# Kernel tuning notes

Measured on AMD Instinct MI355X. Metric: run time of the kernel, lower is better.

## Reference

```python
import jax, jax.numpy as jnp
import numpy as np

HEADS = 16
HEAD_DIM = 64
TOKEN_DIM = 1024
INNER = HEADS * HEAD_DIM


def setup_inputs() -> dict:
    key = jax.random.key(0)
    k1, k2, k3, k4 = jax.random.split(key, 4)
    x = jax.random.normal(k1, (2, 2048, TOKEN_DIM), dtype=jnp.float32)
    # nn.Linear(token_dim, inner*3, bias=False): weight [3*inner, token_dim]
    w_qkv = jax.random.normal(k2, (3 * INNER, TOKEN_DIM), dtype=jnp.float32) * (TOKEN_DIM ** -0.5)
    # nn.Linear(inner, token_dim): weight [token_dim, inner], bias [token_dim]
    w_out = jax.random.normal(k3, (TOKEN_DIM, INNER), dtype=jnp.float32) * (INNER ** -0.5)
    b_out = jax.random.normal(k4, (TOKEN_DIM,), dtype=jnp.float32) * 0.01
    return {"x": x, "w_qkv": w_qkv, "w_out": w_out, "b_out": b_out}


def reference(x, w_qkv, w_out, b_out):
    b, n, _ = x.shape
    scale = HEAD_DIM ** -0.5
    qkv = x @ w_qkv.T                                  # [b, n, 3*inner]
    q, k, v = jnp.split(qkv, 3, axis=-1)
    def split_heads(t):
        return t.reshape(b, n, HEADS, HEAD_DIM).transpose(0, 2, 1, 3)  # [b,h,n,d]
    q, k, v = split_heads(q), split_heads(k), split_heads(v)
    dot = jnp.einsum('bhtd,bhsd->bhts', q, k) * scale  # [b,h,n,n]
    attn = jax.nn.softmax(dot, axis=-1)
    out = jnp.einsum('bhts,bhsd->bhtd', attn, v)       # [b,h,n,d]
    out = out.transpose(0, 2, 1, 3).reshape(b, n, INNER)
    return out @ w_out.T + b_out
```

## Files before the change

### kernel.cpp

```cpp
#include <hip/hip_runtime.h>
#include <hip/hip_bf16.h>

typedef short short4v __attribute__((ext_vector_type(4)));
typedef short short8 __attribute__((ext_vector_type(8)));
typedef float float4v __attribute__((ext_vector_type(4)));

#define HEADS 16
#define HDIM 64
#define TOKDIM 1024
#define SEQ 2048
#define BATCH 2
#define BH (BATCH*HEADS)
#define MROWS (BATCH*SEQ)

__device__ __forceinline__ short f2b(float f) {
    __hip_bfloat16 h = __float2bfloat16(f);
    return *reinterpret_cast<short*>(&h);
}
__device__ __forceinline__ float b2f(short s) {
    __hip_bfloat16 h;
    *reinterpret_cast<short*>(&h) = s;
    return __bfloat162float(h);
}
__device__ __forceinline__ short8 load8_f32_bf16(const float* __restrict__ p) {
    float4v a = *(const float4v*)p;
    float4v b = *(const float4v*)(p + 4);
    short8 r;
    r[0]=f2b(a[0]); r[1]=f2b(a[1]); r[2]=f2b(a[2]); r[3]=f2b(a[3]);
    r[4]=f2b(b[0]); r[5]=f2b(b[1]); r[6]=f2b(b[2]); r[7]=f2b(b[3]);
    return r;
}
__device__ __forceinline__ int packrn(float a, float b) {
    unsigned ua = __float_as_uint(a) + 0x8000u;
    unsigned ub = __float_as_uint(b) + 0x8000u;
    return (int)__builtin_amdgcn_perm(ub, ua, 0x07060302u);
}
__device__ __forceinline__ float hexp2(float x) {
    return __builtin_amdgcn_exp2f(x);
}

__device__ __forceinline__ void stage16(const void* g, void* l) {
    __builtin_amdgcn_global_load_lds((const __attribute__((address_space(1))) void*)g,
                                     (__attribute__((address_space(3))) void*)l, 16, 0, 0);
}

__global__ __launch_bounds__(256)
void cvt_bf16(const float* __restrict__ x,  short* __restrict__ xb,  int n8x,
              const float* __restrict__ wq, short* __restrict__ wqb, int n8q,
              const float* __restrict__ wo, short* __restrict__ wob, int n8o)
{
    int i = blockIdx.x*256 + threadIdx.x;
    const float* s; short* d; int off;
    if (i < n8x)                  { s = x;  d = xb;  off = i; }
    else if (i < n8x + n8q)       { s = wq; d = wqb; off = i - n8x; }
    else if (i < n8x + n8q + n8o) { s = wo; d = wob; off = i - n8x - n8q; }
    else return;
    *(short8*)&d[(size_t)off*8] = load8_f32_bf16(&s[(size_t)off*8]);
}

template<int ABF16>
__global__ __launch_bounds__(256)
void gemm_qkv(const void* __restrict__ Ap, const short* __restrict__ Wq,
              short* __restrict__ Qo, short* __restrict__ Ko, short* __restrict__ Vto)
{
    __shared__ __align__(16) short As[128*32];
    __shared__ __align__(16) short Bs[128*32];
    const int tid  = threadIdx.x;
    const int lane = tid & 63;
    const int wave = tid >> 6;
    const int wm = wave >> 1, wn = wave & 1;
    const int m0 = blockIdx.x * 128;
    const int n0 = blockIdx.y * 128;
    const int col16 = lane & 15, quad = lane >> 4;

    const int srow = lane >> 2;
    const int scol = (lane & 3) * 8;

    float4v acc[4][4];
    #pragma unroll
    for (int i=0;i<4;i++)
        #pragma unroll
        for (int j=0;j<4;j++) acc[i][j] = (float4v){0.f,0.f,0.f,0.f};

    for (int k0 = 0; k0 < TOKDIM; k0 += 32) {
        __syncthreads();
        if (ABF16) {
            const short* A = (const short*)Ap;
            #pragma unroll
            for (int j=0;j<2;++j) {
                const int rb = (wave*2 + j) * 16;
                stage16(&A[(size_t)(m0 + rb + srow)*TOKDIM + k0 + scol], &As[rb*32]);
            }
        } else {
            const float* A = (const float*)Ap;
            #pragma unroll
            for (int s=0;s<2;++s) {
                int blk = tid + s*256;
                int r = blk >> 2, kb = blk & 3;
                *(short8*)&As[r*32 + kb*8] = load8_f32_bf16(&A[(size_t)(m0+r)*TOKDIM + k0 + kb*8]);
            }
        }
        #pragma unroll
        for (int j=0;j<2;++j) {
            const int rb = (wave*2 + j) * 16;
            stage16(&Wq[(size_t)(n0 + rb + srow)*TOKDIM + k0 + scol], &Bs[rb*32]);
        }
        __syncthreads();

        short8 af[4], bfr[4];
        #pragma unroll
        for (int i=0;i<4;i++) af[i]  = *(const short8*)&As[(wm*64 + i*16 + col16)*32 + quad*8];
        #pragma unroll
        for (int j=0;j<4;j++) bfr[j] = *(const short8*)&Bs[(wn*64 + j*16 + col16)*32 + quad*8];
        #pragma unroll
        for (int i=0;i<4;i++)
            #pragma unroll
            for (int j=0;j<4;j++)
                acc[i][j] = __builtin_amdgcn_mfma_f32_16x16x32_bf16(af[i], bfr[j], acc[i][j], 0,0,0);
    }

    #pragma unroll
    for (int i=0;i<4;i++)
        #pragma unroll
        for (int j=0;j<4;j++) {
            const int n = n0 + wn*64 + j*16 + col16;
            const int part = n >> 10;
            const int h = (n & 1023) >> 6;
            const int d = n & 63;
            const int mb = m0 + wm*64 + i*16 + quad*4;
            const int b = mb >> 11;
            const int t = mb & 2047;
            if (part == 2) {
                union { short4v s; int2 i2; } w;
                #pragma unroll
                for (int r=0;r<4;r++) w.s[r] = f2b(acc[i][j][r]);
                *(int2*)&Vto[((size_t)(b*HEADS + h)*HDIM + d)*SEQ + t] = w.i2;
            } else {
                short* dst = (part == 0) ? Qo : Ko;
                #pragma unroll
                for (int r=0;r<4;r++)
                    dst[((size_t)(b*HEADS + h)*SEQ + t + r)*HDIM + d] = f2b(acc[i][j][r]);
            }
        }
}

__global__ __launch_bounds__(256)
void gemm_out(const short* __restrict__ A, const short* __restrict__ W,
              const float* __restrict__ bias, float* __restrict__ C)
{
    __shared__ __align__(16) short As[64*32];
    __shared__ __align__(16) short Bs[128*32];
    const int tid  = threadIdx.x;
    const int lane = tid & 63;
    const int wave = tid >> 6;
    const int wm = wave >> 1, wn = wave & 1;
    const int m0 = blockIdx.x * 64;
    const int n0 = blockIdx.y * 128;
    const int col16 = lane & 15, quad = lane >> 4;

    const int srow = lane >> 2;
    const int scol = (lane & 3) * 8;

    float4v acc[2][4];
    #pragma unroll
    for (int i=0;i<2;i++)
        #pragma unroll
        for (int j=0;j<4;j++) acc[i][j] = (float4v){0.f,0.f,0.f,0.f};

    for (int k0 = 0; k0 < TOKDIM; k0 += 32) {
        __syncthreads();
        {
            const int rb = wave * 16;
            stage16(&A[(size_t)(m0 + rb + srow)*TOKDIM + k0 + scol], &As[rb*32]);
        }
        #pragma unroll
        for (int j=0;j<2;++j) {
            const int rb = (wave*2 + j) * 16;
            stage16(&W[(size_t)(n0 + rb + srow)*TOKDIM + k0 + scol], &Bs[rb*32]);
        }
        __syncthreads();

        short8 af[2], bfr[4];
        #pragma unroll
        for (int i=0;i<2;i++) af[i]  = *(const short8*)&As[(wm*32 + i*16 + col16)*32 + quad*8];
        #pragma unroll
        for (int j=0;j<4;j++) bfr[j] = *(const short8*)&Bs[(wn*64 + j*16 + col16)*32 + quad*8];
        #pragma unroll
        for (int i=0;i<2;i++)
            #pragma unroll
            for (int j=0;j<4;j++)
                acc[i][j] = __builtin_amdgcn_mfma_f32_16x16x32_bf16(af[i], bfr[j], acc[i][j], 0,0,0);
    }

    #pragma unroll
    for (int i=0;i<2;i++)
        #pragma unroll
        for (int j=0;j<4;j++) {
            const int n = n0 + wn*64 + j*16 + col16;
            const float bn = bias[n];
            #pragma unroll
            for (int r=0;r<4;r++) {
                const int m = m0 + wm*32 + i*16 + quad*4 + r;
                C[(size_t)m*TOKDIM + n] = acc[i][j][r] + bn;
            }
        }
}

#define AQB 128
#define KT  64
#define VLD 72

__global__ __launch_bounds__(256, 4)
void attn_kernel(const short* __restrict__ Q, const short* __restrict__ K,
                 const short* __restrict__ Vt, short* __restrict__ AO)
{
    __shared__ __align__(16) short Ks[2][KT*VLD];
    __shared__ __align__(16) short Vs[2][HDIM*VLD];

    const int tid   = threadIdx.x;
    const int lane  = tid & 63;
    const int wave  = tid >> 6;
    const int col16 = lane & 15, quad = lane >> 4;
    const int bh = blockIdx.y;
    const int qb = blockIdx.x*AQB + wave*32;

    const short* Qb = Q  + (size_t)bh*SEQ*HDIM;
    const short* Kb = K  + (size_t)bh*SEQ*HDIM;
    const short* Vb = Vt + (size_t)bh*HDIM*SEQ;

    const int sr = tid >> 2;
    const int sc = (tid & 3) * 16;
    const int rho = sr & 31;
    const int kslot = (sr & 32) + ((rho & 4) << 2) + ((rho & 24) >> 1) + (rho & 3);

    const float qscale = 0.125f * 1.44269504088896f;
    short8 qf[2][2];
    #pragma unroll
    for (int qg=0; qg<2; ++qg)
        #pragma unroll
        for (int kh=0; kh<2; ++kh) {
            short8 raw = *(const short8*)&Qb[(size_t)(qb+qg*16+col16)*HDIM + kh*32 + quad*8];
            #pragma unroll
            for (int j=0;j<8;++j) raw[j] = f2b(b2f(raw[j]) * qscale);
            qf[qg][kh] = raw;
        }

    float4v o[2][4];
    #pragma unroll
    for (int qg=0;qg<2;qg++)
        #pragma unroll
        for (int dt=0;dt<4;dt++) o[qg][dt] = (float4v){0.f,0.f,0.f,0.f};
    float lsum[2] = {0.f, 0.f};

    {
        short8 k0 = *(const short8*)&Kb[(size_t)sr*HDIM + sc];
        short8 k1 = *(const short8*)&Kb[(size_t)sr*HDIM + sc + 8];
        short8 v0 = *(const short8*)&Vb[(size_t)sr*SEQ + sc];
        short8 v1 = *(const short8*)&Vb[(size_t)sr*SEQ + sc + 8];
        *(short8*)&Ks[0][kslot*VLD + sc]     = k0;
        *(short8*)&Ks[0][kslot*VLD + sc + 8] = k1;
        *(short8*)&Vs[0][sr*VLD + sc]        = v0;
        *(short8*)&Vs[0][sr*VLD + sc + 8]    = v1;
    }
    __syncthreads();

    const int NT = SEQ / KT;
    for (int tile = 0; tile < NT; ++tile) {
        const int buf = tile & 1;

        short8 nk0, nk1, nv0, nv1;
        const bool more = (tile + 1 < NT);
        if (more) {
            const int s1 = (tile + 1) * KT;
            nk0 = *(const short8*)&Kb[(size_t)(s1 + sr)*HDIM + sc];
            nk1 = *(const short8*)&Kb[(size_t)(s1 + sr)*HDIM + sc + 8];
            nv0 = *(const short8*)&Vb[(size_t)sr*SEQ + s1 + sc];
            nv1 = *(const short8*)&Vb[(size_t)sr*SEQ + s1 + sc + 8];
        }

        #pragma unroll
        for (int kk = 0; kk < 2; ++kk) {
            short8 ka[2][2];
            #pragma unroll
            for (int nt=0; nt<2; ++nt)
                #pragma unroll
                for (int kh=0; kh<2; ++kh)
                    ka[nt][kh] = *(const short8*)&Ks[buf][(kk*32 + nt*16 + col16)*VLD + kh*32 + quad*8];
            short8 va[4];
            #pragma unroll
            for (int dt=0; dt<4; ++dt)
                va[dt] = *(const short8*)&Vs[buf][(dt*16 + col16)*VLD + kk*32 + quad*8];

            #pragma unroll
            for (int qg=0; qg<2; ++qg) {
                float4v st[2];
                #pragma unroll
                for (int nt=0; nt<2; ++nt) {
                    float4v z = (float4v){0.f,0.f,0.f,0.f};
                    z = __builtin_amdgcn_mfma_f32_16x16x32_bf16(ka[nt][0], qf[qg][0], z, 0,0,0);
                    z = __builtin_amdgcn_mfma_f32_16x16x32_bf16(ka[nt][1], qf[qg][1], z, 0,0,0);
                    st[nt] = z;
                }
                union { int i[4]; short8 s8; } pb;
                float p00 = hexp2(st[0][0]), p01 = hexp2(st[0][1]);
                float p02 = hexp2(st[0][2]), p03 = hexp2(st[0][3]);
                float p10 = hexp2(st[1][0]), p11 = hexp2(st[1][1]);
                float p12 = hexp2(st[1][2]), p13 = hexp2(st[1][3]);
                lsum[qg] += ((p00+p01) + (p02+p03)) + ((p10+p11) + (p12+p13));
                pb.i[0] = packrn(p00, p01); pb.i[1] = packrn(p02, p03);
                pb.i[2] = packrn(p10, p11); pb.i[3] = packrn(p12, p13);

                #pragma unroll
                for (int dt=0; dt<4; ++dt)
                    o[qg][dt] = __builtin_amdgcn_mfma_f32_16x16x32_bf16(va[dt], pb.s8, o[qg][dt], 0,0,0);
            }
        }

        if (more) {
            const int nb = buf ^ 1;
            *(short8*)&Ks[nb][kslot*VLD + sc]     = nk0;
            *(short8*)&Ks[nb][kslot*VLD + sc + 8] = nk1;
            *(short8*)&Vs[nb][sr*VLD + sc]        = nv0;
            *(short8*)&Vs[nb][sr*VLD + sc + 8]    = nv1;
        }
        __syncthreads();
    }

    #pragma unroll
    for (int qg=0; qg<2; ++qg) {
        lsum[qg] += __shfl_xor(lsum[qg], 16);
        lsum[qg] += __shfl_xor(lsum[qg], 32);
    }

    const int b = bh >> 4, h = bh & 15;
    #pragma unroll
    for (int qg=0; qg<2; ++qg) {
        const float inv = 1.0f / lsum[qg];
        const int t = qb + qg*16 + col16;
        #pragma unroll
        for (int dt=0; dt<4; ++dt) {
            union { short4v s; int2 i2; } w;
            #pragma unroll
            for (int r=0;r<4;++r) w.s[r] = f2b(o[qg][dt][r] * inv);
            *(int2*)&AO[((size_t)(b*SEQ + t))*TOKDIM + h*64 + dt*16 + quad*4] = w.i2;
        }
    }
}

extern "C" void kernel_launch(void* const* d_in, const int* in_sizes, int n_in,
                              void* d_out, int out_size, void* d_ws, size_t ws_size,
                              hipStream_t stream)
{
    const float* x    = (const float*)d_in[0];
    const float* wqkv = (const float*)d_in[1];
    const float* wout = (const float*)d_in[2];
    const float* bout = (const float*)d_in[3];
    float* out = (float*)d_out;

    char* ws = (char*)d_ws;
    const size_t SZ   = (size_t)BH*SEQ*HDIM*sizeof(short);
    const size_t WQB  = (size_t)3*TOKDIM*TOKDIM*sizeof(short);
    const size_t WOB  = (size_t)TOKDIM*TOKDIM*sizeof(short);
    const size_t NEED_FULL = SZ + WQB + WOB + 3*SZ;
    const bool full = ws_size >= NEED_FULL;

    short *Xb, *Wqb, *Wob, *Qt, *Kt, *Vt, *AO;
    if (full) {
        Xb  = (short*)ws;
        Wqb = (short*)(ws + SZ);
        Wob = (short*)(ws + SZ + WQB);
        Qt  = (short*)(ws + SZ + WQB + WOB);
        Kt  = Qt + SZ/2;
        Vt  = Kt + SZ/2;
        AO  = Xb;
    } else {
        Xb  = nullptr;
        Wqb = (short*)ws;
        Wob = (short*)(ws + WQB);
        Qt  = (short*)(ws + WQB + WOB);
        Kt  = Qt + SZ/2;
        Vt  = Kt + SZ/2;
        AO  = Vt + SZ/2;
    }

    const int n8x = full ? (BATCH*SEQ*TOKDIM)/8 : 0;
    const int n8q = (3*TOKDIM*TOKDIM)/8;
    const int n8o = (TOKDIM*TOKDIM)/8;
    const int cvt_blocks = (n8x + n8q + n8o + 255) / 256;
    cvt_bf16<<<cvt_blocks, 256, 0, stream>>>(x, Xb, n8x, wqkv, Wqb, n8q, wout, Wob, n8o);

    if (full)
        gemm_qkv<1><<<dim3(MROWS/128, (3*TOKDIM)/128), 256, 0, stream>>>(
            (const void*)Xb, Wqb, Qt, Kt, Vt);
    else
        gemm_qkv<0><<<dim3(MROWS/128, (3*TOKDIM)/128), 256, 0, stream>>>(
            (const void*)x, Wqb, Qt, Kt, Vt);

    attn_kernel<<<dim3(SEQ/AQB, BH), 256, 0, stream>>>(Qt, Kt, Vt, AO);

    gemm_out<<<dim3(MROWS/64, TOKDIM/128), 256, 0, stream>>>(AO, Wob, bout, out);
}
```

Before: 184.6 us.

## Split KV sequence across wave pairs in attention with 64-query waves and LDS merge

Each attention block now has two wave pairs. Each pair processes half of the key/value sequence, and each wave handles 64 queries instead of 32. This doubles the reuse of every K/V fragment loaded from LDS across query groups. Double buffering is replaced by a single buffer per half, with two barriers per tile. The partial outputs and row sums are merged through LDS at the end. Register pressure rises (launch bounds drop to 2 blocks per SM), and the load-to-compute overlap is weaker because of the extra barrier.

```diff
diff --git a/kernel.cpp b/kernel.cpp
--- a/kernel.cpp
+++ b/kernel.cpp
@@ -209,73 +209,77 @@
 #define AQB 128
 #define KT  64
 #define VLD 72
-
-__global__ __launch_bounds__(256, 4)
+#define NTH 16
+
+__global__ __launch_bounds__(256, 2)
 void attn_kernel(const short* __restrict__ Q, const short* __restrict__ K,
                  const short* __restrict__ Vt, short* __restrict__ AO)
 {
-    __shared__ __align__(16) short Ks[2][KT*VLD];
-    __shared__ __align__(16) short Vs[2][HDIM*VLD];
+    __shared__ __align__(16) short SL[2*2*KT*VLD];
 
     const int tid   = threadIdx.x;
     const int lane  = tid & 63;
     const int wave  = tid >> 6;
     const int col16 = lane & 15, quad = lane >> 4;
-    const int bh = blockIdx.y;
-    const int qb = blockIdx.x*AQB + wave*32;
+    const int bh  = blockIdx.y;
+    const int qh  = wave & 1;
+    const int kh2 = wave >> 1;
+    const int qb  = blockIdx.x*AQB + qh*64;
 
     const short* Qb = Q  + (size_t)bh*SEQ*HDIM;
     const short* Kb = K  + (size_t)bh*SEQ*HDIM;
     const short* Vb = Vt + (size_t)bh*HDIM*SEQ;
 
-    const int sr = tid >> 2;
-    const int sc = (tid & 3) * 16;
+    short* Kcs = &SL[kh2*2*KT*VLD];
+    short* Vcs = Kcs + KT*VLD;
+
+    const int local = tid & 127;
+    const int sr = local >> 1;
+    const int sc = (local & 1) * 32;
     const int rho = sr & 31;
     const int kslot = (sr & 32) + ((rho & 4) << 2) + ((rho & 24) >> 1) + (rho & 3);
+    const int kbase = kh2 * 1024;
 
     const float qscale = 0.125f * 1.44269504088896f;
-    short8 qf[2][2];
-    #pragma unroll
-    for (int qg=0; qg<2; ++qg)
-        #pragma unroll
-        for (int kh=0; kh<2; ++kh) {
-            short8 raw = *(const short8*)&Qb[(size_t)(qb+qg*16+col16)*HDIM + kh*32 + quad*8];
+    short8 qf[4][2];
+    #pragma unroll
+    for (int qg=0; qg<4; ++qg)
+        #pragma unroll
+        for (int kk=0; kk<2; ++kk) {
+            short8 raw = *(const short8*)&Qb[(size_t)(qb+qg*16+col16)*HDIM + kk*32 + quad*8];
             #pragma unroll
             for (int j=0;j<8;++j) raw[j] = f2b(b2f(raw[j]) * qscale);
-            qf[qg][kh] = raw;
-        }
-
-    float4v o[2][4];
-    #pragma unroll
-    for (int qg=0;qg<2;qg++)
+            qf[qg][kk] = raw;
+        }
+
+    float4v o[4][4];
+    #pragma unroll
+    for (int qg=0;qg<4;qg++)
         #pragma unroll
         for (int dt=0;dt<4;dt++) o[qg][dt] = (float4v){0.f,0.f,0.f,0.f};
-    float lsum[2] = {0.f, 0.f};
+    float lsum[4] = {0.f,0.f,0.f,0.f};
 
     {
-        short8 k0 = *(const short8*)&Kb[(size_t)sr*HDIM + sc];
-        short8 k1 = *(const short8*)&Kb[(size_t)sr*HDIM + sc + 8];
-        short8 v0 = *(const short8*)&Vb[(size_t)sr*SEQ + sc];
-        short8 v1 = *(const short8*)&Vb[(size_t)sr*SEQ + sc + 8];
-        *(short8*)&Ks[0][kslot*VLD + sc]     = k0;
-        *(short8*)&Ks[0][kslot*VLD + sc + 8] = k1;
-        *(short8*)&Vs[0][sr*VLD + sc]        = v0;
-        *(short8*)&Vs[0][sr*VLD + sc + 8]    = v1;
+        #pragma unroll
+        for (int i=0;i<4;++i) {
+            *(short8*)&Kcs[kslot*VLD + sc + i*8] =
+                *(const short8*)&Kb[(size_t)(kbase + sr)*HDIM + sc + i*8];
+            *(short8*)&Vcs[sr*VLD + sc + i*8] =
+                *(const short8*)&Vb[(size_t)sr*SEQ + kbase + sc + i*8];
+        }
     }
     __syncthreads();
 
-    const int NT = SEQ / KT;
-    for (int tile = 0; tile < NT; ++tile) {
-        const int buf = tile & 1;
-
-        short8 nk0, nk1, nv0, nv1;
-        const bool more = (tile + 1 < NT);
+    for (int t = 0; t < NTH; ++t) {
+        short8 nk[4], nv[4];
+        const bool more = (t + 1 < NTH);
         if (more) {
-            const int s1 = (tile + 1) * KT;
-            nk0 = *(const short8*)&Kb[(size_t)(s1 + sr)*HDIM + sc];
-            nk1 = *(const short8*)&Kb[(size_t)(s1 + sr)*HDIM + sc + 8];
-            nv0 = *(const short8*)&Vb[(size_t)sr*SEQ + s1 + sc];
-            nv1 = *(const short8*)&Vb[(size_t)sr*SEQ + s1 + sc + 8];
+            const int g1 = kbase + (t+1)*KT;
+            #pragma unroll
+            for (int i=0;i<4;++i) {
+                nk[i] = *(const short8*)&Kb[(size_t)(g1 + sr)*HDIM + sc + i*8];
+                nv[i] = *(const short8*)&Vb[(size_t)sr*SEQ + g1 + sc + i*8];
+            }
         }
 
         #pragma unroll
@@ -285,14 +289,14 @@
             for (int nt=0; nt<2; ++nt)
                 #pragma unroll
                 for (int kh=0; kh<2; ++kh)
-                    ka[nt][kh] = *(const short8*)&Ks[buf][(kk*32 + nt*16 + col16)*VLD + kh*32 + quad*8];
+                    ka[nt][kh] = *(const short8*)&Kcs[(kk*32 + nt*16 + col16)*VLD + kh*32 + quad*8];
             short8 va[4];
             #pragma unroll
             for (int dt=0; dt<4; ++dt)
-                va[dt] = *(const short8*)&Vs[buf][(dt*16 + col16)*VLD + kk*32 + quad*8];
-
-            #pragma unroll
-            for (int qg=0; qg<2; ++qg) {
+                va[dt] = *(const short8*)&Vcs[(dt*16 + col16)*VLD + kk*32 + quad*8];
+
+            #pragma unroll
+            for (int qg=0; qg<4; ++qg) {
                 float4v st[2];
                 #pragma unroll
                 for (int nt=0; nt<2; ++nt) {
@@ -316,33 +320,50 @@
             }
         }
 
+        __syncthreads();
         if (more) {
-            const int nb = buf ^ 1;
-            *(short8*)&Ks[nb][kslot*VLD + sc]     = nk0;
-            *(short8*)&Ks[nb][kslot*VLD + sc + 8] = nk1;
-            *(short8*)&Vs[nb][sr*VLD + sc]        = nv0;
-            *(short8*)&Vs[nb][sr*VLD + sc + 8]    = nv1;
-        }
-        __syncthreads();
-    }
-
-    #pragma unroll
-    for (int qg=0; qg<2; ++qg) {
+            #pragma unroll
+            for (int i=0;i<4;++i) {
+                *(short8*)&Kcs[kslot*VLD + sc + i*8] = nk[i];
+                *(short8*)&Vcs[sr*VLD + sc + i*8]    = nv[i];
+            }
+            __syncthreads();
+        }
+    }
+
+    #pragma unroll
+    for (int qg=0; qg<4; ++qg) {
         lsum[qg] += __shfl_xor(lsum[qg], 16);
         lsum[qg] += __shfl_xor(lsum[qg], 32);
     }
 
-    const int b = bh >> 4, h = bh & 15;
-    #pragma unroll
-    for (int qg=0; qg<2; ++qg) {
-        const float inv = 1.0f / lsum[qg];
-        const int t = qb + qg*16 + col16;
-        #pragma unroll
-        for (int dt=0; dt<4; ++dt) {
-            union { short4v s; int2 i2; } w;
-            #pragma unroll
-            for (int r=0;r<4;++r) w.s[r] = f2b(o[qg][dt][r] * inv);
-            *(int2*)&AO[((size_t)(b*SEQ + t))*TOKDIM + h*64 + dt*16 + quad*4] = w.i2;
+    float* M = (float*)SL;
+    float* Mw = M + (qh*64 + lane)*68;
+    if (kh2 == 1) {
+        #pragma unroll
+        for (int qg=0; qg<4; ++qg) {
+            #pragma unroll
+            for (int dt=0; dt<4; ++dt)
+                *(float4v*)&Mw[(qg*4+dt)*4] = o[qg][dt];
+            Mw[64+qg] = lsum[qg];
+        }
+    }
+    __syncthreads();
+    if (kh2 == 0) {
+        const int b = bh >> 4, h = bh & 15;
+        #pragma unroll
+        for (int qg=0; qg<4; ++qg) {
+            lsum[qg] += Mw[64+qg];
+            const float inv = 1.0f / lsum[qg];
+            const int tq = qb + qg*16 + col16;
+            #pragma unroll
+            for (int dt=0; dt<4; ++dt) {
+                float4v ov = o[qg][dt] + *(const float4v*)&Mw[(qg*4+dt)*4];
+                union { short4v s; int2 i2; } w;
+                #pragma unroll
+                for (int r=0;r<4;++r) w.s[r] = f2b(ov[r] * inv);
+                *(int2*)&AO[((size_t)(b*SEQ + tq))*TOKDIM + h*64 + dt*16 + quad*4] = w.i2;
+            }
         }
     }
 }
```

New measurement: 178.7 us. 3.2% less time.
